# Kernel tuning notes

Measured on AMD Instinct MI355X. Metric: run time of the kernel, lower is better.

Reference implementation:

```python
import jax, jax.numpy as jnp
import numpy as np

N_HEAD = 16
BLOCK_SIZE = 2049  # w2 last dim = block_size - 1 = 2048


def setup_inputs() -> dict:
    key = jax.random.key(0)
    ks = jax.random.split(key, 9)
    B, T, C = 2, 2048, 1024
    hd = C // N_HEAD
    M = BLOCK_SIZE - 1
    return {
        "x": jax.random.normal(ks[0], (B, T, C), jnp.float32),
        "w1_w": jax.random.normal(ks[1], (C, C), jnp.float32) * 0.02,
        "w1_b": jax.random.normal(ks[2], (C,), jnp.float32) * 0.02,
        # torch uniform_(a=-0.001, b=0.001)
        "w2": jax.random.uniform(ks[3], (N_HEAD, hd, M), jnp.float32, -0.001, 0.001),
        "b2": jax.random.normal(ks[4], (M,), jnp.float32) * 0.02,
        "value_w": jax.random.normal(ks[5], (C, C), jnp.float32) * 0.02,
        "value_b": jax.random.normal(ks[6], (C,), jnp.float32) * 0.02,
        "proj_w": jax.random.normal(ks[7], (C, C), jnp.float32) * 0.02,
        "proj_b": jax.random.normal(ks[8], (C,), jnp.float32) * 0.02,
    }


def reference(x, w1_w, w1_b, w2, b2, value_w, value_b, proj_w, proj_b):
    B, T, C = x.shape
    H = N_HEAD
    hd = C // H
    M = w2.shape[-1]  # block_size - 1
    # kernel = relu(w1(x)), split heads -> [B, H, T, hd]
    k = jax.nn.relu(x @ w1_w.T + w1_b).reshape(B, T, H, hd).transpose(0, 2, 1, 3)
    # synthesizer scores: [B, H, T, M]
    attn = jnp.einsum('bhtd,hdm->bhtm', k, w2) + b2
    # causal mask = tril(ones(block,block))[:T, :M] == 0 -> -inf
    causal = jnp.tril(jnp.ones((T, M), dtype=bool))
    attn = jnp.where(causal, attn, -jnp.inf)
    # softmax over first T score columns
    attn = jax.nn.softmax(attn[..., :T], axis=-1)  # [B, H, T, T]
    v = (x @ value_w.T + value_b).reshape(B, T, H, hd).transpose(0, 2, 1, 3)
    out = jnp.einsum('bhts,bhsd->bhtd', attn, v)
    out = out.transpose(0, 2, 1, 3).reshape(B, T, C)
    return out @ proj_w.T + proj_b
```

## Files before the change

kernel.cpp:

```cpp
#include <hip/hip_runtime.h>
#include <math.h>
#include <stdint.h>

typedef __bf16 bf16;
typedef __bf16 bf16x8 __attribute__((ext_vector_type(8)));
typedef __bf16 bf16x4 __attribute__((ext_vector_type(4)));
typedef float f32x4 __attribute__((ext_vector_type(4)));
typedef unsigned int u32;

__device__ __forceinline__ int swz(int row, int chunk) {
    return row * 64 + ((chunk ^ (row & 7)) << 3);
}

__device__ __forceinline__ void gld16(void* lds, const void* g) {
    __builtin_amdgcn_global_load_lds(
        (const __attribute__((address_space(1))) u32*)g,
        (__attribute__((address_space(3))) u32*)lds, 16, 0, 0);
}

__device__ __forceinline__ void stage8(bf16* dst, const bf16* src, size_t srcStride,
                                       int w, int l) {
    const int br = w * 8;
    const int r = br + (l >> 3);
    const int gs = (l & 7) ^ (r & 7);
    gld16(dst + br * 64, src + (size_t)r * srcStride + gs * 8);
}

__global__ void cast_bf16_k(const float* __restrict__ src, bf16* __restrict__ dst, int n) {
    const int stride = gridDim.x * blockDim.x * 4;
    for (int i = (blockIdx.x * blockDim.x + threadIdx.x) * 4; i < n; i += stride) {
        float4 v = *(const float4*)(src + i);
        bf16x4 o = {(bf16)v.x, (bf16)v.y, (bf16)v.z, (bf16)v.w};
        *(bf16x4*)(dst + i) = o;
    }
}

__global__ void cast3_bf16_k(const float* __restrict__ s0, bf16* __restrict__ d0,
                             const float* __restrict__ s1, bf16* __restrict__ d1,
                             const float* __restrict__ s2, bf16* __restrict__ d2, int n) {
    const int stride = gridDim.x * blockDim.x * 4;
    for (int i = (blockIdx.x * blockDim.x + threadIdx.x) * 4; i < n; i += stride) {
        float4 v0 = *(const float4*)(s0 + i);
        float4 v1 = *(const float4*)(s1 + i);
        float4 v2 = *(const float4*)(s2 + i);
        bf16x4 o0 = {(bf16)v0.x, (bf16)v0.y, (bf16)v0.z, (bf16)v0.w};
        bf16x4 o1 = {(bf16)v1.x, (bf16)v1.y, (bf16)v1.z, (bf16)v1.w};
        bf16x4 o2 = {(bf16)v2.x, (bf16)v2.y, (bf16)v2.z, (bf16)v2.w};
        *(bf16x4*)(d0 + i) = o0;
        *(bf16x4*)(d1 + i) = o1;
        *(bf16x4*)(d2 + i) = o2;
    }
}

__global__ __launch_bounds__(256) void w2_transpose_k(const float* __restrict__ w2,
                                                      bf16* __restrict__ w2t, int M) {
    __shared__ float Tf[64][65];
    const int h = blockIdx.y, m0 = blockIdx.x * 64, t = threadIdx.x;
    {
        const int dr = t >> 4, c4 = (t & 15) * 4;
        #pragma unroll
        for (int it = 0; it < 4; ++it) {
            const int d = dr + it * 16;
            float4 v = *(const float4*)(w2 + ((size_t)h * 64 + d) * M + m0 + c4);
            Tf[d][c4] = v.x; Tf[d][c4 + 1] = v.y; Tf[d][c4 + 2] = v.z; Tf[d][c4 + 3] = v.w;
        }
    }
    __syncthreads();
    const int m = t >> 2;
    #pragma unroll
    for (int it = 0; it < 2; ++it) {
        const int ch = (t & 3) + it * 4;
        bf16x8 o;
        #pragma unroll
        for (int j = 0; j < 8; ++j) o[j] = (bf16)Tf[ch * 8 + j][m];
        *(bf16x8*)(w2t + ((size_t)h * M + m0 + m) * 64 + ch * 8) = o;
    }
}

__global__ __launch_bounds__(256, 2) void gemm_bf16_k(const bf16* __restrict__ A,
                                                   const bf16* __restrict__ Bw,
                                                   const float* __restrict__ bias,
                                                   const float* __restrict__ bias2,
                                                   float* __restrict__ C0,
                                                   bf16* __restrict__ CK,
                                                   bf16* __restrict__ CV,
                                                   int M, int N, int K, int mode, int Ns)
{
    __shared__ __align__(16) bf16 As[2][128 * 64];
    __shared__ __align__(16) bf16 Bs[2][128 * 64];
    const int tid = threadIdx.x;
    const int w = tid >> 6, l = tid & 63;
    const int wr = w >> 1, wc = w & 1;
    const int lc = l & 15, lg = l >> 4;
    const int row0 = blockIdx.y * 128, col0 = blockIdx.x * 128;

    f32x4 acc[4][4] = {};

    const int nk = K >> 6;
    auto issue = [&](int buf, int k0) {
        #pragma unroll
        for (int i = 0; i < 4; ++i) {
            const int br = (w * 4 + i) * 8;
            const int r = br + (l >> 3);
            const int gs = (l & 7) ^ (r & 7);
            gld16(&As[buf][br * 64], A  + (size_t)(row0 + r) * K + k0 + gs * 8);
            gld16(&Bs[buf][br * 64], Bw + (size_t)(col0 + r) * K + k0 + gs * 8);
        }
    };

    issue(0, 0);
    int cur = 0;
    for (int kt = 0; kt < nk; ++kt) {
        if (kt + 1 < nk) {
            issue(cur ^ 1, (kt + 1) << 6);
            asm volatile("s_waitcnt vmcnt(8)" ::: "memory");
        } else {
            asm volatile("s_waitcnt vmcnt(0)" ::: "memory");
        }
        __builtin_amdgcn_s_barrier();
        #pragma unroll
        for (int ks = 0; ks < 2; ++ks) {
            bf16x8 af[4], bfv[4];
            #pragma unroll
            for (int i = 0; i < 4; ++i) {
                af[i]  = *(const bf16x8*)&As[cur][swz(wr * 64 + i * 16 + lc, ks * 4 + lg)];
                bfv[i] = *(const bf16x8*)&Bs[cur][swz(wc * 64 + i * 16 + lc, ks * 4 + lg)];
            }
            #pragma unroll
            for (int mi = 0; mi < 4; ++mi)
                #pragma unroll
                for (int ni = 0; ni < 4; ++ni)
                    acc[mi][ni] = __builtin_amdgcn_mfma_f32_16x16x32_bf16(af[mi], bfv[ni], acc[mi][ni], 0, 0, 0);
        }
        asm volatile("s_waitcnt lgkmcnt(0)" ::: "memory");
        __builtin_amdgcn_s_barrier();
        cur ^= 1;
    }

    #pragma unroll
    for (int ni = 0; ni < 4; ++ni) {
        const int col = col0 + wc * 64 + ni * 16 + lc;
        #pragma unroll
        for (int mi = 0; mi < 4; ++mi) {
            const int rowb = row0 + wr * 64 + mi * 16 + lg * 4;
            f32x4 v = acc[mi][ni];
            if (mode == 0) {
                const float bv = bias[col];
                #pragma unroll
                for (int r = 0; r < 4; ++r)
                    C0[(size_t)(rowb + r) * N + col] = v[r] + bv;
            } else if (col < Ns) {
                const float bv = bias[col];
                #pragma unroll
                for (int r = 0; r < 4; ++r)
                    CK[(size_t)(rowb + r) * Ns + col] = (bf16)fmaxf(v[r] + bv, 0.f);
            } else {
                const float bv = bias2[col - Ns];
                const int b = rowb >> 11, tt = rowb & 2047;
                bf16x4 o = {(bf16)(v[0] + bv), (bf16)(v[1] + bv),
                            (bf16)(v[2] + bv), (bf16)(v[3] + bv)};
                *(bf16x4*)(CV + ((size_t)b * Ns + (col - Ns)) * 2048 + tt) = o;
            }
        }
    }
}

__device__ __forceinline__ void tile_step(bf16x8 kf0, bf16x8 kf1,
                                          const bf16* Wb, const bf16* Vb,
                                          bf16* Pw, const float* b2l, int s0,
                                          f32x4 (&acc)[4], float& lsum,
                                          bool diag, int lc, int lg, int wq)
{
    f32x4 sv[4];
    #pragma unroll
    for (int st = 0; st < 4; ++st) {
        const float4 b4 = *(const float4*)&b2l[s0 + st * 16 + lg * 4];
        sv[st] = {b4.x, b4.y, b4.z, b4.w};
    }
    #pragma unroll
    for (int st = 0; st < 4; ++st) {
        bf16x8 wb0 = *(const bf16x8*)&Wb[swz(st * 16 + lc, lg)];
        bf16x8 wb1 = *(const bf16x8*)&Wb[swz(st * 16 + lc, 4 + lg)];
        sv[st] = __builtin_amdgcn_mfma_f32_16x16x32_bf16(wb0, kf0, sv[st], 0, 0, 0);
        sv[st] = __builtin_amdgcn_mfma_f32_16x16x32_bf16(wb1, kf1, sv[st], 0, 0, 0);
    }
    const int qv = wq * 16 + lc;
    #pragma unroll
    for (int st = 0; st < 4; ++st) {
        float e[4];
        #pragma unroll
        for (int r = 0; r < 4; ++r) {
            const int sidx = st * 16 + lg * 4 + r;
            float ev = __expf(sv[st][r]);
            if (diag && sidx > qv) ev = 0.f;
            e[r] = ev;
            lsum += ev;
        }
        bf16x4 pw = {(bf16)e[0], (bf16)e[1], (bf16)e[2], (bf16)e[3]};
        const int chunk = st * 2 + (lg >> 1);
        *(bf16x4*)&Pw[lc * 64 + ((chunk ^ (lc & 7)) << 3) + ((lg & 1) << 2)] = pw;
    }
    #pragma unroll
    for (int ks = 0; ks < 2; ++ks) {
        bf16x8 pf = *(const bf16x8*)&Pw[swz(lc, ks * 4 + lg)];
        #pragma unroll
        for (int dt = 0; dt < 4; ++dt) {
            bf16x8 vv = *(const bf16x8*)&Vb[swz(dt * 16 + lc, ks * 4 + lg)];
            acc[dt] = __builtin_amdgcn_mfma_f32_16x16x32_bf16(pf, vv, acc[dt], 0, 0, 0);
        }
    }
}

__global__ __launch_bounds__(512, 4) void synth_attn_v9(const bf16* __restrict__ Kb,
                                                        const bf16* __restrict__ VT,
                                                        const bf16* __restrict__ w2t,
                                                        const float* __restrict__ b2,
                                                        bf16* __restrict__ Ob)
{
    constexpr int T = 2048, C = 1024, M = 2048;
    __shared__ __align__(16) bf16 Wl[3][64 * 64];
    __shared__ __align__(16) bf16 Vl[3][64 * 64];
    __shared__ __align__(16) bf16 Pl[8][16 * 64];
    __shared__ float b2l[M];
    const int tid = threadIdx.x;
    const int w = tid >> 6, l = tid & 63;
    const int lc = l & 15, lg = l >> 4;
    const int wq = w & 3, wt = w >> 2;

    const int bx = blockIdx.x;
    const int j = bx & 15;
    const int bh = bx >> 4;
    const int h = bh & 15, b = bh >> 4;
    const int tA = j, tB = 31 - j;
    const int myT = wt ? tA : tB;
    const int t0 = myT * 64;

    *(float4*)&b2l[tid * 4] = *(const float4*)(b2 + tid * 4);
    __syncthreads();

    const bf16* Wgt = w2t + (size_t)h * M * 64;
    const bf16* Vgt = VT + ((size_t)b * C + h * 64) * T;
    bf16* Pw = &Pl[w][0];

    const bf16* Kg = Kb + (size_t)(b * T + t0 + wq * 16 + lc) * C + h * 64;
    const bf16x8 kf0 = *(const bf16x8*)(Kg + lg * 8);
    const bf16x8 kf1 = *(const bf16x8*)(Kg + 32 + lg * 8);

    stage8(&Wl[0][0], Wgt, 64, w, l);
    stage8(&Vl[0][0], Vgt, T, w, l);
    stage8(&Wl[1][0], Wgt + (size_t)64 * 64, 64, w, l);
    stage8(&Vl[1][0], Vgt + 64, T, w, l);

    f32x4 acc[4] = {};
    float lsum = 0.f;

    int cur = 0;
    for (int sb = 0; sb <= tB; ++sb) {
        const int s0 = sb * 64;
        if (sb < tB) asm volatile("s_waitcnt vmcnt(2)" ::: "memory");
        else         asm volatile("s_waitcnt vmcnt(0)" ::: "memory");
        __builtin_amdgcn_s_barrier();

        if (sb <= myT)
            tile_step(kf0, kf1, &Wl[cur][0], &Vl[cur][0], Pw, b2l, s0,
                      acc, lsum, sb == myT, lc, lg, wq);

        if (sb + 2 <= tB) {
            int nx = cur + 2; if (nx >= 3) nx -= 3;
            stage8(&Wl[nx][0], Wgt + (size_t)(s0 + 128) * 64, 64, w, l);
            stage8(&Vl[nx][0], Vgt + (s0 + 128), T, w, l);
        }
        if (++cur == 3) cur = 0;
    }

    float ls = lsum;
    ls += __shfl_xor(ls, 16);
    ls += __shfl_xor(ls, 32);
    #pragma unroll
    for (int r = 0; r < 4; ++r) {
        const float inv = 1.f / __shfl(ls, lg * 4 + r);
        bf16* dst = Ob + (size_t)(b * T + t0 + wq * 16 + lg * 4 + r) * C + h * 64;
        #pragma unroll
        for (int dt = 0; dt < 4; ++dt)
            dst[dt * 16 + lc] = (bf16)(acc[dt][r] * inv);
    }
}

extern "C" void kernel_launch(void* const* d_in, const int* in_sizes, int n_in,
                              void* d_out, int out_size, void* d_ws, size_t ws_size,
                              hipStream_t stream) {
    const float* x       = (const float*)d_in[0];
    const float* w1_w    = (const float*)d_in[1];
    const float* w1_b    = (const float*)d_in[2];
    const float* w2      = (const float*)d_in[3];
    const float* b2      = (const float*)d_in[4];
    const float* value_w = (const float*)d_in[5];
    const float* value_b = (const float*)d_in[6];
    const float* proj_w  = (const float*)d_in[7];
    const float* proj_b  = (const float*)d_in[8];

    const int B = 2, T = 2048, C = 1024, H = 16, M = 2048;
    const int R = B * T;

    bf16* xb  = (bf16*)d_ws;
    bf16* w1b = xb  + (size_t)R * C;
    bf16* vwb = w1b + (size_t)C * C;
    bf16* w2t = vwb + (size_t)C * C;
    bf16* pwb = w2t + (size_t)H * M * 64;
    bf16* Kb  = pwb + (size_t)C * C;
    bf16* VTb = Kb  + (size_t)R * C;
    bf16* Ob  = VTb + (size_t)R * C;

    cast_bf16_k<<<1024, 256, 0, stream>>>(x, xb, R * C);
    cast3_bf16_k<<<512, 256, 0, stream>>>(w1_w, w1b, value_w, vwb, proj_w, pwb, C * C);
    w2_transpose_k<<<dim3(M / 64, H), 256, 0, stream>>>(w2, w2t, M);

    gemm_bf16_k<<<dim3(2 * C / 128, R / 128), 256, 0, stream>>>(
        xb, w1b, w1_b, value_b, nullptr, Kb, VTb, R, 2 * C, C, 1, C);

    synth_attn_v9<<<dim3(512), 512, 0, stream>>>(Kb, VTb, w2t, b2, Ob);

    gemm_bf16_k<<<dim3(C / 128, R / 128), 256, 0, stream>>>(
        Ob, pwb, proj_b, nullptr, (float*)d_out, nullptr, nullptr, R, C, C, 0, C);
}
```

Baseline: 103.2 us.

## Switch synthesizer attention to 32x32x16 MFMA with register-resident P tiles

Measured after the change: 113.7 us. 10.1% more time.

```diff
diff --git a/kernel.cpp b/kernel.cpp
--- a/kernel.cpp
+++ b/kernel.cpp
@@ -6,6 +6,7 @@
 typedef __bf16 bf16x8 __attribute__((ext_vector_type(8)));
 typedef __bf16 bf16x4 __attribute__((ext_vector_type(4)));
 typedef float f32x4 __attribute__((ext_vector_type(4)));
+typedef float f32x16 __attribute__((ext_vector_type(16)));
 typedef unsigned int u32;
 
 __device__ __forceinline__ int swz(int row, int chunk) {
@@ -18,12 +19,15 @@
         (__attribute__((address_space(3))) u32*)lds, 16, 0, 0);
 }
 
-__device__ __forceinline__ void stage8(bf16* dst, const bf16* src, size_t srcStride,
-                                       int w, int l) {
-    const int br = w * 8;
-    const int r = br + (l >> 3);
-    const int gs = (l & 7) ^ (r & 7);
-    gld16(dst + br * 64, src + (size_t)r * srcStride + gs * 8);
+__device__ __forceinline__ void stage16(bf16* dst, const bf16* src, size_t srcStride,
+                                        int w, int l) {
+    #pragma unroll
+    for (int i = 0; i < 2; ++i) {
+        const int br = w * 16 + i * 8;
+        const int r = br + (l >> 3);
+        const int gs = (l & 7) ^ (r & 7);
+        gld16(dst + br * 64, src + (size_t)r * srcStride + gs * 8);
+    }
 }
 
 __global__ void cast_bf16_k(const float* __restrict__ src, bf16* __restrict__ dst, int n) {
@@ -165,124 +169,143 @@
     }
 }
 
-__device__ __forceinline__ void tile_step(bf16x8 kf0, bf16x8 kf1,
-                                          const bf16* Wb, const bf16* Vb,
-                                          bf16* Pw, const float* b2l, int s0,
-                                          f32x4 (&acc)[4], float& lsum,
-                                          bool diag, int lc, int lg, int wq)
-{
-    f32x4 sv[4];
-    #pragma unroll
-    for (int st = 0; st < 4; ++st) {
-        const float4 b4 = *(const float4*)&b2l[s0 + st * 16 + lg * 4];
-        sv[st] = {b4.x, b4.y, b4.z, b4.w};
-    }
-    #pragma unroll
-    for (int st = 0; st < 4; ++st) {
-        bf16x8 wb0 = *(const bf16x8*)&Wb[swz(st * 16 + lc, lg)];
-        bf16x8 wb1 = *(const bf16x8*)&Wb[swz(st * 16 + lc, 4 + lg)];
-        sv[st] = __builtin_amdgcn_mfma_f32_16x16x32_bf16(wb0, kf0, sv[st], 0, 0, 0);
-        sv[st] = __builtin_amdgcn_mfma_f32_16x16x32_bf16(wb1, kf1, sv[st], 0, 0, 0);
-    }
-    const int qv = wq * 16 + lc;
-    #pragma unroll
-    for (int st = 0; st < 4; ++st) {
-        float e[4];
-        #pragma unroll
-        for (int r = 0; r < 4; ++r) {
-            const int sidx = st * 16 + lg * 4 + r;
-            float ev = __expf(sv[st][r]);
-            if (diag && sidx > qv) ev = 0.f;
-            e[r] = ev;
-            lsum += ev;
-        }
-        bf16x4 pw = {(bf16)e[0], (bf16)e[1], (bf16)e[2], (bf16)e[3]};
-        const int chunk = st * 2 + (lg >> 1);
-        *(bf16x4*)&Pw[lc * 64 + ((chunk ^ (lc & 7)) << 3) + ((lg & 1) << 2)] = pw;
-    }
-    #pragma unroll
-    for (int ks = 0; ks < 2; ++ks) {
-        bf16x8 pf = *(const bf16x8*)&Pw[swz(lc, ks * 4 + lg)];
-        #pragma unroll
-        for (int dt = 0; dt < 4; ++dt) {
-            bf16x8 vv = *(const bf16x8*)&Vb[swz(dt * 16 + lc, ks * 4 + lg)];
-            acc[dt] = __builtin_amdgcn_mfma_f32_16x16x32_bf16(pf, vv, acc[dt], 0, 0, 0);
-        }
-    }
-}
-
-__global__ __launch_bounds__(512, 4) void synth_attn_v9(const bf16* __restrict__ Kb,
-                                                        const bf16* __restrict__ VT,
-                                                        const bf16* __restrict__ w2t,
-                                                        const float* __restrict__ b2,
-                                                        bf16* __restrict__ Ob)
+__global__ __launch_bounds__(256, 2) void synth_attn_v10(const bf16* __restrict__ Kb,
+                                                         const bf16* __restrict__ VT,
+                                                         const bf16* __restrict__ w2t,
+                                                         const float* __restrict__ b2,
+                                                         bf16* __restrict__ Ob)
 {
     constexpr int T = 2048, C = 1024, M = 2048;
     __shared__ __align__(16) bf16 Wl[3][64 * 64];
     __shared__ __align__(16) bf16 Vl[3][64 * 64];
-    __shared__ __align__(16) bf16 Pl[8][16 * 64];
     __shared__ float b2l[M];
     const int tid = threadIdx.x;
     const int w = tid >> 6, l = tid & 63;
-    const int lc = l & 15, lg = l >> 4;
-    const int wq = w & 3, wt = w >> 2;
+    const int c = l & 31, hi = l >> 5;
 
     const int bx = blockIdx.x;
-    const int j = bx & 15;
-    const int bh = bx >> 4;
+    const int hseg = bx >> 8, idx = bx & 255;
+    const int jj = idx & 15;
+    const int a = hseg ? (15 - jj) : jj;
+    const int bh = (hseg << 4) | (idx >> 4);
     const int h = bh & 15, b = bh >> 4;
-    const int tA = j, tB = 31 - j;
-    const int myT = wt ? tA : tB;
-    const int t0 = myT * 64;
-
-    *(float4*)&b2l[tid * 4] = *(const float4*)(b2 + tid * 4);
+    const int tA = a, tB = 31 - a;
+    const int myT = (w >> 1) ? tA : tB;
+    const int t0w = myT * 64 + (w & 1) * 32;
+
+    *(float4*)&b2l[tid * 8]     = *(const float4*)(b2 + tid * 8);
+    *(float4*)&b2l[tid * 8 + 4] = *(const float4*)(b2 + tid * 8 + 4);
     __syncthreads();
 
     const bf16* Wgt = w2t + (size_t)h * M * 64;
     const bf16* Vgt = VT + ((size_t)b * C + h * 64) * T;
-    bf16* Pw = &Pl[w][0];
-
-    const bf16* Kg = Kb + (size_t)(b * T + t0 + wq * 16 + lc) * C + h * 64;
-    const bf16x8 kf0 = *(const bf16x8*)(Kg + lg * 8);
-    const bf16x8 kf1 = *(const bf16x8*)(Kg + 32 + lg * 8);
-
-    stage8(&Wl[0][0], Wgt, 64, w, l);
-    stage8(&Vl[0][0], Vgt, T, w, l);
-    stage8(&Wl[1][0], Wgt + (size_t)64 * 64, 64, w, l);
-    stage8(&Vl[1][0], Vgt + 64, T, w, l);
-
-    f32x4 acc[4] = {};
+
+    const bf16* Kg = Kb + (size_t)(b * T + t0w + c) * C + h * 64 + hi * 8;
+    bf16x8 kf[4];
+    #pragma unroll
+    for (int kst = 0; kst < 4; ++kst) kf[kst] = *(const bf16x8*)(Kg + kst * 16);
+
+    stage16(&Wl[0][0], Wgt, 64, w, l);
+    stage16(&Vl[0][0], Vgt, T, w, l);
+    stage16(&Wl[1][0], Wgt + (size_t)64 * 64, 64, w, l);
+    stage16(&Vl[1][0], Vgt + 64, T, w, l);
+
+    f32x16 o0 = {}, o1 = {};
     float lsum = 0.f;
 
     int cur = 0;
     for (int sb = 0; sb <= tB; ++sb) {
         const int s0 = sb * 64;
-        if (sb < tB) asm volatile("s_waitcnt vmcnt(2)" ::: "memory");
+        if (sb < tB) asm volatile("s_waitcnt vmcnt(4)" ::: "memory");
         else         asm volatile("s_waitcnt vmcnt(0)" ::: "memory");
         __builtin_amdgcn_s_barrier();
 
-        if (sb <= myT)
-            tile_step(kf0, kf1, &Wl[cur][0], &Vl[cur][0], Pw, b2l, s0,
-                      acc, lsum, sb == myT, lc, lg, wq);
+        if (sb <= myT) {
+            const bf16* Wb = &Wl[cur][0];
+            const bf16* Vb = &Vl[cur][0];
+
+            f32x16 sv0, sv1;
+            #pragma unroll
+            for (int qd = 0; qd < 4; ++qd) {
+                float4 b4 = *(const float4*)&b2l[s0 + qd * 8 + 4 * hi];
+                float4 b5 = *(const float4*)&b2l[s0 + 32 + qd * 8 + 4 * hi];
+                sv0[4*qd] = b4.x; sv0[4*qd+1] = b4.y; sv0[4*qd+2] = b4.z; sv0[4*qd+3] = b4.w;
+                sv1[4*qd] = b5.x; sv1[4*qd+1] = b5.y; sv1[4*qd+2] = b5.z; sv1[4*qd+3] = b5.w;
+            }
+            #pragma unroll
+            for (int kst = 0; kst < 4; ++kst) {
+                bf16x8 w0 = *(const bf16x8*)&Wb[swz(c,      kst * 2 + hi)];
+                bf16x8 w1 = *(const bf16x8*)&Wb[swz(32 + c, kst * 2 + hi)];
+                sv0 = __builtin_amdgcn_mfma_f32_32x32x16_bf16(w0, kf[kst], sv0, 0, 0, 0);
+                sv1 = __builtin_amdgcn_mfma_f32_32x32x16_bf16(w1, kf[kst], sv1, 0, 0, 0);
+            }
+
+            const bool diag = (sb == myT);
+            const int qv = (w & 1) * 32 + c;
+            u32 U0[8], U1[8];
+            #pragma unroll
+            for (int qd = 0; qd < 4; ++qd) {
+                float e0[4], e1[4];
+                #pragma unroll
+                for (int k = 0; k < 4; ++k) {
+                    const int sbase = qd * 8 + 4 * hi + k;
+                    float ev0 = __expf(sv0[4*qd + k]);
+                    float ev1 = __expf(sv1[4*qd + k]);
+                    if (diag && sbase > qv)      ev0 = 0.f;
+                    if (diag && sbase + 32 > qv) ev1 = 0.f;
+                    lsum += ev0 + ev1;
+                    e0[k] = ev0; e1[k] = ev1;
+                }
+                union { bf16x4 v; u32 u[2]; } p0, p1;
+                p0.v = {(bf16)e0[0], (bf16)e0[1], (bf16)e0[2], (bf16)e0[3]};
+                p1.v = {(bf16)e1[0], (bf16)e1[1], (bf16)e1[2], (bf16)e1[3]};
+                U0[2*qd] = p0.u[0]; U0[2*qd+1] = p0.u[1];
+                U1[2*qd] = p1.u[0]; U1[2*qd+1] = p1.u[1];
+            }
+
+            #define PV_TILE(Uarr, st)                                              \
+            {                                                                      \
+                _Pragma("unroll")                                                  \
+                for (int kk = 0; kk < 2; ++kk) {                                   \
+                    u32 A00 = Uarr[4*kk],   A01 = Uarr[4*kk+1];                    \
+                    u32 A10 = Uarr[4*kk+2], A11 = Uarr[4*kk+3];                    \
+                    u32 s00 = (u32)__shfl_xor((int)A00, 32);                       \
+                    u32 s01 = (u32)__shfl_xor((int)A01, 32);                       \
+                    u32 s10 = (u32)__shfl_xor((int)A10, 32);                       \
+                    u32 s11 = (u32)__shfl_xor((int)A11, 32);                       \
+                    union { u32 u[4]; bf16x8 v; } pa;                              \
+                    pa.u[0] = hi ? s10 : A00;                                      \
+                    pa.u[1] = hi ? s11 : A01;                                      \
+                    pa.u[2] = hi ? A10 : s00;                                      \
+                    pa.u[3] = hi ? A11 : s01;                                      \
+                    const int ch = (st) * 4 + kk * 2 + hi;                         \
+                    bf16x8 v0 = *(const bf16x8*)&Vb[swz(c,      ch)];              \
+                    bf16x8 v1 = *(const bf16x8*)&Vb[swz(32 + c, ch)];              \
+                    o0 = __builtin_amdgcn_mfma_f32_32x32x16_bf16(pa.v, v0, o0, 0, 0, 0); \
+                    o1 = __builtin_amdgcn_mfma_f32_32x32x16_bf16(pa.v, v1, o1, 0, 0, 0); \
+                }                                                                  \
+            }
+            PV_TILE(U0, 0)
+            PV_TILE(U1, 1)
+            #undef PV_TILE
+        }
 
         if (sb + 2 <= tB) {
             int nx = cur + 2; if (nx >= 3) nx -= 3;
-            stage8(&Wl[nx][0], Wgt + (size_t)(s0 + 128) * 64, 64, w, l);
-            stage8(&Vl[nx][0], Vgt + (s0 + 128), T, w, l);
+            stage16(&Wl[nx][0], Wgt + (size_t)(s0 + 128) * 64, 64, w, l);
+            stage16(&Vl[nx][0], Vgt + (s0 + 128), T, w, l);
         }
         if (++cur == 3) cur = 0;
     }
 
-    float ls = lsum;
-    ls += __shfl_xor(ls, 16);
-    ls += __shfl_xor(ls, 32);
-    #pragma unroll
-    for (int r = 0; r < 4; ++r) {
-        const float inv = 1.f / __shfl(ls, lg * 4 + r);
-        bf16* dst = Ob + (size_t)(b * T + t0 + wq * 16 + lg * 4 + r) * C + h * 64;
-        #pragma unroll
-        for (int dt = 0; dt < 4; ++dt)
-            dst[dt * 16 + lc] = (bf16)(acc[dt][r] * inv);
+    const float inv = 1.f / (lsum + __shfl_xor(lsum, 32));
+    #pragma unroll
+    for (int r = 0; r < 16; ++r) {
+        const int q_ = (r & 3) + 8 * (r >> 2) + 4 * hi;
+        const float iv = __shfl(inv, q_);
+        bf16* dst = Ob + (size_t)(b * T + t0w + q_) * C + h * 64;
+        dst[c]      = (bf16)(o0[r] * iv);
+        dst[32 + c] = (bf16)(o1[r] * iv);
     }
 }
 
@@ -318,7 +341,7 @@
     gemm_bf16_k<<<dim3(2 * C / 128, R / 128), 256, 0, stream>>>(
         xb, w1b, w1_b, value_b, nullptr, Kb, VTb, R, 2 * C, C, 1, C);
 
-    synth_attn_v9<<<dim3(512), 512, 0, stream>>>(Kb, VTb, w2t, b2, Ob);
+    synth_attn_v10<<<dim3(512), 256, 0, stream>>>(Kb, VTb, w2t, b2, Ob);
 
     gemm_bf16_k<<<dim3(C / 128, R / 128), 256, 0, stream>>>(
         Ob, pwb, proj_b, nullptr, (float*)d_out, nullptr, nullptr, R, C, C, 0, C);
```
